# Optimization experiments

Measured on AMD Instinct MI355X. Metric: run time of the kernel, lower is better.

Reference implementation:

```python
import jax, jax.numpy as jnp
import numpy as np

L = 4        # num_layers
N = 50000    # nodes
E = 500000   # edges
B = 32       # graphs
H = 64       # hidden_dim
HP = 16      # hidden_dim_pe
P = 8        # pe_dim
BN_EPS = 1e-5


def setup_inputs() -> dict:
    key = jax.random.key(0)
    ks = jax.random.split(key, 22)
    nrm = lambda k, s: jax.random.normal(k, s, dtype=jnp.float32)
    w = lambda k, s: nrm(k, s) * 0.1
    return {
        'x': nrm(ks[0], (N, H)),
        'pe': nrm(ks[1], (N, P)),
        'Lambda': jax.random.uniform(ks[2], (B, P), dtype=jnp.float32),
        'edge_attr': nrm(ks[3], (E, H)),
        'edge_index': jax.random.randint(ks[4], (2, E), 0, N),
        'batch': jnp.sort(jax.random.randint(ks[5], (N,), 0, B)),
        # edge encoder (SPE): eigenvalue MLP + output projection
        'We1': w(ks[6], (L, P, HP * P)), 'be1': jnp.zeros((L, HP * P)),
        'Wee': w(ks[7], (L, HP, H)),     'bee': jnp.zeros((L, H)),
        # GINE mlp: Linear-BN-ReLU-Linear
        'W1': w(ks[8], (L, H, H)), 'b1': jnp.zeros((L, H)),
        'g1': jnp.ones((L, H)),    'beta1': jnp.zeros((L, H)),
        'W2': w(ks[9], (L, H, H)), 'b2': jnp.zeros((L, H)),
        # equivariant PE conv: edge gate + channel Linear
        'Wg': w(ks[10], (L, H, HP)),  'bg': jnp.zeros((L, HP)),
        'Wp': w(ks[11], (L, HP, HP)), 'bp': jnp.zeros((L, HP)),
        # outer BatchNorm per layer
        'gn': jnp.ones((L, H)), 'bnb': jnp.zeros((L, H)),
    }


def _bn(h, gamma, beta):
    mu = h.mean(0)
    var = h.var(0)
    return gamma * (h - mu) * jax.lax.rsqrt(var + BN_EPS) + beta


def reference(x, pe, Lambda, edge_attr, We1, be1, Wee, bee, W1, b1, g1, beta1,
              W2, b2, Wg, bg, Wp, bp, gn, bnb, edge_index, batch):
    src, dst = edge_index[0], edge_index[1]
    bsrc = batch[src]                       # [E] graph id of source node
    z = jnp.tile(pe[:, None, :], (1, HP, 1))  # [N, HP, P]
    for i in range(L):
        # SPE edge encoder: phi(Lambda)-weighted inner product over pe axis
        phi = jax.nn.relu(Lambda @ We1[i] + be1[i]).reshape(B, HP, P)
        eh = jnp.einsum('ehp,ehp->eh', phi[bsrc] * z[src], z[dst])  # [E, HP]
        ea = eh @ Wee[i] + bee[i] + edge_attr                       # [E, H]
        # GINEConv: scatter-add of relu(x_src + edge_attr), eps = 0
        agg = jax.ops.segment_sum(jax.nn.relu(x[src] + ea), dst, num_segments=N)
        h = x + agg
        h = jax.nn.relu(_bn(h @ W1[i] + b1[i], g1[i], beta1[i])) @ W2[i] + b2[i]
        # GINConvEquivariant: gated scatter-add, Linear on channel axis
        gate = jax.nn.relu(ea @ Wg[i] + bg[i])                      # [E, HP]
        msgz = jax.nn.relu(z[src] + gate[:, :, None])               # [E, HP, P]
        z = z + jax.ops.segment_sum(msgz, dst, num_segments=N)
        z = jnp.einsum('nhp,hk->nkp', z, Wp[i]) + bp[i][None, :, None]
        x = _bn(h, gn[i], bnb[i])
        if i != L - 1:
            x = jax.nn.relu(x)
    return x, z
```

## Files before the change

### kernel.cpp

```cpp
#include <hip/hip_runtime.h>

#define NN 50000
#define EE 500000
#define LL 4

typedef unsigned short u16;
typedef unsigned int u32;

__device__ __forceinline__ float bfc(u16 u) { return __uint_as_float(((u32)u) << 16); }
__device__ __forceinline__ u16 f2bf(float f) {
    u32 u = __float_as_uint(f);
    return (u16)((u + 0x7fffu + ((u >> 16) & 1u)) >> 16);
}
__device__ __forceinline__ float lanebc(float v, int l) {
    return __int_as_float(__builtin_amdgcn_readlane(__float_as_int(v), l));
}
__device__ __forceinline__ void unpack2(u32 w, float& lo, float& hi) {
    lo = __uint_as_float(w << 16);
    hi = __uint_as_float(w & 0xffff0000u);
}

__global__ __launch_bounds__(256) void k_init(const float* __restrict__ x, float* __restrict__ Xf,
                                              int* __restrict__ deg, int* __restrict__ cursor) {
    for (int i = blockIdx.x * 256 + threadIdx.x; i < NN * 64; i += gridDim.x * 256)
        Xf[i] = x[i];
    for (int i = blockIdx.x * 256 + threadIdx.x; i < NN; i += gridDim.x * 256) {
        deg[i] = 0;
        cursor[i] = 0;
    }
}

__global__ __launch_bounds__(128) void k_phi(const float* __restrict__ Lam, const float* __restrict__ We1,
                                             const float* __restrict__ be1, float* __restrict__ phiA) {
    int l = blockIdx.x >> 5, b = blockIdx.x & 31, j = threadIdx.x;
    float acc = be1[l * 128 + j];
    for (int q = 0; q < 8; q++)
        acc = fmaf(Lam[b * 8 + q], We1[l * 1024 + q * 128 + j], acc);
    phiA[l * 4096 + b * 128 + j] = fmaxf(acc, 0.f);
}

__global__ __launch_bounds__(256) void k_small(const float* __restrict__ Wee, const float* __restrict__ Wg,
                                               float* __restrict__ MA) {
    int l = blockIdx.x, t = threadIdx.x;
    int k = t >> 4, h = t & 15;
    float m = 0.f;
    for (int f = 0; f < 64; f++)
        m = fmaf(Wee[l * 1024 + k * 64 + f], Wg[l * 1024 + f * 16 + h], m);
    MA[l * 256 + t] = m;
}

__global__ __launch_bounds__(256) void k_hist(const int* __restrict__ ei, int* __restrict__ deg) {
    int e = blockIdx.x * 256 + threadIdx.x;
    if (e < EE) {
        int d = ei[EE + e];
        if (d >= 0 && d < NN) atomicAdd(&deg[d], 1);
    }
}

__global__ __launch_bounds__(256) void k_scan1(const int* __restrict__ deg, int* __restrict__ rowptr,
                                               int* __restrict__ bsum) {
    __shared__ int tmp[256];
    int t = threadIdx.x, i = blockIdx.x * 256 + t;
    int v = (i < NN) ? deg[i] : 0;
    tmp[t] = v;
    __syncthreads();
    for (int off = 1; off < 256; off <<= 1) {
        int a = (t >= off) ? tmp[t - off] : 0;
        __syncthreads();
        tmp[t] += a;
        __syncthreads();
    }
    if (i < NN) rowptr[i] = tmp[t] - v;
    if (t == 255) bsum[blockIdx.x] = tmp[255];
}

__global__ __launch_bounds__(256) void k_scan2(const int* __restrict__ bsum, int* __restrict__ boff,
                                               int* __restrict__ rowptr, int nb) {
    __shared__ int tmp[256];
    int t = threadIdx.x;
    int v = (t < nb) ? bsum[t] : 0;
    tmp[t] = v;
    __syncthreads();
    for (int off = 1; off < 256; off <<= 1) {
        int a = (t >= off) ? tmp[t - off] : 0;
        __syncthreads();
        tmp[t] += a;
        __syncthreads();
    }
    if (t < nb) boff[t] = tmp[t] - v;
    if (t == 255) rowptr[NN] = tmp[255];
}

__global__ __launch_bounds__(256) void k_scan3(int* __restrict__ rowptr, const int* __restrict__ boff) {
    int i = blockIdx.x * 256 + threadIdx.x;
    if (i < NN) rowptr[i] += boff[blockIdx.x];
}

__global__ __launch_bounds__(256) void k_scatter(const int* __restrict__ ei, const int* __restrict__ batch,
                                                 const int* __restrict__ rowptr, int* __restrict__ cursor,
                                                 u32* __restrict__ sb, int* __restrict__ eeo) {
    int e = blockIdx.x * 256 + threadIdx.x;
    if (e < EE) {
        int s = ei[e], d = ei[EE + e];
        if (s < 0) s = 0; if (s >= NN) s = NN - 1;
        if (d < 0) d = 0; if (d >= NN) d = NN - 1;
        int pos = rowptr[d] + atomicAdd(&cursor[d], 1);
        if (pos >= 0 && pos < EE) {
            sb[pos] = (u32)s | ((u32)(batch[s] & 31) << 16);
            eeo[pos] = e;
        }
    }
}

__global__ __launch_bounds__(256) void k_perm(const float* __restrict__ eat, const int* __restrict__ eeo,
                                              u16* __restrict__ eatp) {
    for (long long i = (long long)blockIdx.x * 256 + threadIdx.x; i < (long long)EE * 64;
         i += (long long)gridDim.x * 256) {
        int idx = (int)(i >> 6), j = (int)(i & 63);
        int e = eeo[idx];
        eatp[i] = f2bf(eat[(size_t)e * 64 + j]);
    }
}

__global__ __launch_bounds__(256) void k_eag2(const u16* __restrict__ eatp, const float* __restrict__ WgL,
                                              const float* __restrict__ beeL, const float* __restrict__ bgL,
                                              u32* __restrict__ EAGp) {
    __shared__ float sWg[1024];
    __shared__ float scv[16];
    __shared__ u32 srow[256][33];
    const int t = threadIdx.x;
    for (int i = t; i < 1024; i += 256) sWg[i] = WgL[i];
    __syncthreads();
    if (t < 16) {
        float c = bgL[t];
        for (int j = 0; j < 64; j++) c = fmaf(beeL[j], sWg[j * 16 + t], c);
        scv[t] = c;
    }
    const int base = blockIdx.x * 256;
    const u32* eat32 = (const u32*)eatp;
    for (int i = t; i < 256 * 32; i += 256) {
        int r = i >> 5, c = i & 31;
        int idx = base + r;
        srow[r][c] = (idx < EE) ? eat32[(size_t)idx * 32 + c] : 0u;
    }
    __syncthreads();
    const int idx = base + t;
    if (idx < EE) {
        float acc[16];
#pragma unroll
        for (int h = 0; h < 16; h++) acc[h] = scv[h];
#pragma unroll
        for (int c = 0; c < 32; c++) {
            float a0, a1;
            unpack2(srow[t][c], a0, a1);
            const float* w0 = &sWg[(2 * c) * 16];
#pragma unroll
            for (int h = 0; h < 16; h++) acc[h] = fmaf(a0, w0[h], fmaf(a1, w0[16 + h], acc[h]));
        }
        u32 w[8];
#pragma unroll
        for (int h = 0; h < 8; h++) w[h] = (u32)f2bf(acc[h]) | ((u32)f2bf(acc[8 + h]) << 16);
        uint4* op = reinterpret_cast<uint4*>(EAGp + (size_t)idx * 8);
        op[0] = make_uint4(w[0], w[1], w[2], w[3]);
        op[1] = make_uint4(w[4], w[5], w[6], w[7]);
    }
}

template <int INM>
__global__ __launch_bounds__(256) void k_edge_b(const float* __restrict__ Zf,
                                                const float* __restrict__ pe,
                                                const float* __restrict__ Xf,
                                                const u16* __restrict__ eatp, const u32* __restrict__ EAGp,
                                                const int* __restrict__ rowptr, const u32* __restrict__ sb,
                                                const float* __restrict__ phiL, const float* __restrict__ WeeL,
                                                const float* __restrict__ beeL, const float* __restrict__ ML,
                                                const float* __restrict__ WpL, const float* __restrict__ bpL,
                                                float* __restrict__ Hf, float* __restrict__ ZfO,
                                                double* __restrict__ stats) {
    __shared__ float sphi[32 * 128];
    __shared__ float sWp[256];
    __shared__ float sbp[16];
    if (blockIdx.x == 0) stats[threadIdx.x] = 0.0;
    for (int t = threadIdx.x; t < 4096; t += 256) sphi[t] = phiL[t];
    if (threadIdx.x < 256) sWp[threadIdx.x] = WpL[threadIdx.x];
    if (threadIdx.x < 16) sbp[threadIdx.x] = bpL[threadIdx.x];
    const int lane = threadIdx.x & 63;
    const int wid = threadIdx.x >> 6;
    const int hlo = lane >> 3;
    const int pp = lane & 7;
    float wee[16], mlo[16], mhi[16];
#pragma unroll
    for (int k = 0; k < 16; k++) {
        wee[k] = WeeL[k * 64 + lane];
        mlo[k] = ML[k * 16 + hlo];
        mhi[k] = ML[k * 16 + 8 + hlo];
    }
    const float beev = beeL[lane];
    __syncthreads();
    for (int n = blockIdx.x * 4 + wid; n < NN; n += gridDim.x * 4) {
        float zd0, zd1;
        if (INM == 0) { zd0 = zd1 = pe[n * 8 + pp]; }
        else { zd0 = Zf[n * 128 + lane]; zd1 = Zf[n * 128 + 64 + lane]; }
        float accx = Xf[n * 64 + lane];
        float az0 = zd0, az1 = zd1;
        int i0 = rowptr[n], i1 = rowptr[n + 1];
        if (i0 < 0) i0 = 0;
        if (i1 > EE) i1 = EE;
        u32 w = 0;
        float zs0 = 0.f, zs1 = 0.f, xs = 0.f, eav = 0.f, glo = 0.f, ghi = 0.f;
        if (i0 < i1) {
            w = sb[i0];
            const int s = w & 0xffff;
            if (INM == 0) { zs0 = zs1 = pe[s * 8 + pp]; }
            else { zs0 = Zf[s * 128 + lane]; zs1 = Zf[s * 128 + 64 + lane]; }
            xs = Xf[s * 64 + lane];
            eav = bfc(eatp[(size_t)i0 * 64 + lane]);
            unpack2(EAGp[(size_t)i0 * 8 + hlo], glo, ghi);
        }
        for (int idx = i0; idx < i1; ++idx) {
            const int idxn = (idx + 1 < i1) ? idx + 1 : idx;
            const u32 wn = sb[idxn];
            const int sn = wn & 0xffff;
            float zs0n, zs1n;
            if (INM == 0) { zs0n = zs1n = pe[sn * 8 + pp]; }
            else { zs0n = Zf[sn * 128 + lane]; zs1n = Zf[sn * 128 + 64 + lane]; }
            const float xsn = Xf[sn * 64 + lane];
            const float eavn = bfc(eatp[(size_t)idxn * 64 + lane]);
            float glon, ghin;
            unpack2(EAGp[(size_t)idxn * 8 + hlo], glon, ghin);
            const int b = (w >> 16) & 31;
            float p0 = sphi[b * 128 + lane] * zs0 * zd0;
            float p1 = sphi[b * 128 + 64 + lane] * zs1 * zd1;
            p0 += __shfl_xor(p0, 1); p1 += __shfl_xor(p1, 1);
            p0 += __shfl_xor(p0, 2); p1 += __shfl_xor(p1, 2);
            p0 += __shfl_xor(p0, 4); p1 += __shfl_xor(p1, 4);
            float eaA = 0.f, eaB = 0.f, gloA = glo, gloB = 0.f, ghiA = ghi, ghiB = 0.f;
#pragma unroll
            for (int k = 0; k < 8; k++) {
                const float ehk = lanebc(p0, k << 3);
                eaA = fmaf(ehk, wee[k], eaA);
                gloA = fmaf(ehk, mlo[k], gloA);
                ghiA = fmaf(ehk, mhi[k], ghiA);
            }
#pragma unroll
            for (int k = 0; k < 8; k++) {
                const float ehk = lanebc(p1, k << 3);
                eaB = fmaf(ehk, wee[8 + k], eaB);
                gloB = fmaf(ehk, mlo[8 + k], gloB);
                ghiB = fmaf(ehk, mhi[8 + k], ghiB);
            }
            accx += fmaxf(0.f, xs + (beev + eav + eaA + eaB));
            az0 += fmaxf(0.f, zs0 + fmaxf(gloA + gloB, 0.f));
            az1 += fmaxf(0.f, zs1 + fmaxf(ghiA + ghiB, 0.f));
            w = wn; zs0 = zs0n; zs1 = zs1n; xs = xsn; eav = eavn; glo = glon; ghi = ghin;
        }
        Hf[n * 64 + lane] = accx;
        float r0 = sbp[hlo], r1 = sbp[8 + hlo];
#pragma unroll
        for (int h = 0; h < 8; h++) {
            const float v = __shfl(az0, (h << 3) + pp);
            r0 = fmaf(v, sWp[h * 16 + hlo], r0);
            r1 = fmaf(v, sWp[h * 16 + 8 + hlo], r1);
        }
#pragma unroll
        for (int h = 0; h < 8; h++) {
            const float v = __shfl(az1, (h << 3) + pp);
            r0 = fmaf(v, sWp[(8 + h) * 16 + hlo], r0);
            r1 = fmaf(v, sWp[(8 + h) * 16 + 8 + hlo], r1);
        }
        ZfO[n * 128 + lane] = r0;
        ZfO[n * 128 + 64 + lane] = r1;
    }
}

template <int INM>
__global__ __launch_bounds__(256) void k_edge_s(const float* __restrict__ Zf,
                                                const float* __restrict__ pe,
                                                const float* __restrict__ Xf, const float* __restrict__ eat,
                                                const int* __restrict__ rowptr, const u32* __restrict__ sb,
                                                const int* __restrict__ eeo,
                                                const float* __restrict__ phiL, const float* __restrict__ WeeL,
                                                const float* __restrict__ beeL,
                                                const float* __restrict__ WgL, const float* __restrict__ bgL,
                                                const float* __restrict__ WpL, const float* __restrict__ bpL,
                                                float* __restrict__ Hf, float* __restrict__ ZfO,
                                                double* __restrict__ stats) {
    __shared__ float sphi[32 * 128];
    __shared__ float sWp[256];
    __shared__ float sbp[16];
    if (blockIdx.x == 0) stats[threadIdx.x] = 0.0;
    for (int t = threadIdx.x; t < 4096; t += 256) sphi[t] = phiL[t];
    if (threadIdx.x < 256) sWp[threadIdx.x] = WpL[threadIdx.x];
    if (threadIdx.x < 16) sbp[threadIdx.x] = bpL[threadIdx.x];
    const int lane = threadIdx.x & 63;
    const int wid = threadIdx.x >> 6;
    const int hlo = lane >> 3;
    const int pp = lane & 7;
    const int h16 = lane & 15;
    const int g16 = lane & 48;
    float wee[16], wgr[16];
#pragma unroll
    for (int k = 0; k < 16; k++) {
        wee[k] = WeeL[k * 64 + lane];
        wgr[k] = WgL[(g16 + k) * 16 + h16];
    }
    const float beev = beeL[lane];
    const float bgr = bgL[h16];
    __syncthreads();
    for (int n = blockIdx.x * 4 + wid; n < NN; n += gridDim.x * 4) {
        float zd0, zd1;
        if (INM == 0) { zd0 = zd1 = pe[n * 8 + pp]; }
        else { zd0 = Zf[n * 128 + lane]; zd1 = Zf[n * 128 + 64 + lane]; }
        float accx = Xf[n * 64 + lane];
        float az0 = zd0, az1 = zd1;
        int i0 = rowptr[n], i1 = rowptr[n + 1];
        if (i0 < 0) i0 = 0;
        if (i1 > EE) i1 = EE;
        for (int idx = i0; idx < i1; ++idx) {
            const u32 w = sb[idx];
            const int s = w & 0xffff;
            const int b = (w >> 16) & 31;
            int e = eeo[idx];
            e = (e < 0) ? 0 : ((e >= EE) ? EE - 1 : e);
            float zs0, zs1;
            if (INM == 0) { zs0 = zs1 = pe[s * 8 + pp]; }
            else { zs0 = Zf[s * 128 + lane]; zs1 = Zf[s * 128 + 64 + lane]; }
            float p0 = sphi[b * 128 + lane] * zs0 * zd0;
            float p1 = sphi[b * 128 + 64 + lane] * zs1 * zd1;
            p0 += __shfl_xor(p0, 1); p1 += __shfl_xor(p1, 1);
            p0 += __shfl_xor(p0, 2); p1 += __shfl_xor(p1, 2);
            p0 += __shfl_xor(p0, 4); p1 += __shfl_xor(p1, 4);
            float ea = beev + eat[(size_t)e * 64 + lane];
#pragma unroll
            for (int k = 0; k < 8; k++) ea = fmaf(lanebc(p0, k << 3), wee[k], ea);
#pragma unroll
            for (int k = 0; k < 8; k++) ea = fmaf(lanebc(p1, k << 3), wee[8 + k], ea);
            float gp = 0.f;
#pragma unroll
            for (int i = 0; i < 16; i++) gp = fmaf(__shfl(ea, g16 + i), wgr[i], gp);
            gp += __shfl_xor(gp, 16);
            gp += __shfl_xor(gp, 32);
            const float gv = fmaxf(gp + bgr, 0.f);
            const float glo = __shfl(gv, hlo);
            const float ghi = __shfl(gv, 8 + hlo);
            const float xs = Xf[s * 64 + lane];
            accx += fmaxf(0.f, xs + ea);
            az0 += fmaxf(0.f, zs0 + glo);
            az1 += fmaxf(0.f, zs1 + ghi);
        }
        Hf[n * 64 + lane] = accx;
        float r0 = sbp[hlo], r1 = sbp[8 + hlo];
#pragma unroll
        for (int h = 0; h < 8; h++) {
            const float v = __shfl(az0, (h << 3) + pp);
            r0 = fmaf(v, sWp[h * 16 + hlo], r0);
            r1 = fmaf(v, sWp[h * 16 + 8 + hlo], r1);
        }
#pragma unroll
        for (int h = 0; h < 8; h++) {
            const float v = __shfl(az1, (h << 3) + pp);
            r0 = fmaf(v, sWp[(8 + h) * 16 + hlo], r0);
            r1 = fmaf(v, sWp[(8 + h) * 16 + 8 + hlo], r1);
        }
        ZfO[n * 128 + lane] = r0;
        ZfO[n * 128 + 64 + lane] = r1;
    }
}

__global__ __launch_bounds__(256) void k_gemm1(float* Buf, const float* __restrict__ WL,
                                               const float* __restrict__ bL,
                                               double* __restrict__ sum, double* __restrict__ sq) {
    __shared__ float sW[4096];
    __shared__ double red[512];
    for (int t = threadIdx.x; t < 4096; t += 256) sW[t] = WL[t];
    const int lane = threadIdx.x & 63, wid = threadIdx.x >> 6;
    const float bv = bL[lane];
    __syncthreads();
    double s = 0.0, q = 0.0;
    for (int n = blockIdx.x * 4 + wid; n < NN; n += gridDim.x * 4) {
        const float h = Buf[n * 64 + lane];
        float acc = bv;
#pragma unroll
        for (int k = 0; k < 64; k++) acc = fmaf(lanebc(h, k), sW[k * 64 + lane], acc);
        Buf[n * 64 + lane] = acc;
        s += (double)acc;
        q += (double)acc * (double)acc;
    }
    red[threadIdx.x] = s;
    red[256 + threadIdx.x] = q;
    __syncthreads();
    if (threadIdx.x < 64) {
        s = red[threadIdx.x] + red[threadIdx.x + 64] + red[threadIdx.x + 128] + red[threadIdx.x + 192];
        q = red[256 + threadIdx.x] + red[320 + threadIdx.x] + red[384 + threadIdx.x] + red[448 + threadIdx.x];
        atomicAdd(&sum[lane], s);
        atomicAdd(&sq[lane], q);
    }
}

__global__ __launch_bounds__(256) void k_gemm2(float* Buf, const float* __restrict__ WL,
                                               const float* __restrict__ bL,
                                               const float* __restrict__ gL, const float* __restrict__ betaL,
                                               const double* __restrict__ s1, const double* __restrict__ q1,
                                               double* __restrict__ sum, double* __restrict__ sq) {
    __shared__ float sW[4096];
    __shared__ double red[512];
    for (int t = threadIdx.x; t < 4096; t += 256) sW[t] = WL[t];
    const int lane = threadIdx.x & 63, wid = threadIdx.x >> 6;
    const float bv = bL[lane];
    const double mu = s1[lane] * (1.0 / NN);
    const double var = q1[lane] * (1.0 / NN) - mu * mu;
    const float inv = rsqrtf(fmaxf((float)var, 0.f) + 1e-5f);
    const float gm = gL[lane] * inv;
    const float ga = betaL[lane] - (float)mu * gm;
    __syncthreads();
    double s = 0.0, q = 0.0;
    for (int n = blockIdx.x * 4 + wid; n < NN; n += gridDim.x * 4) {
        const float v = Buf[n * 64 + lane];
        const float r = fmaxf(fmaf(v, gm, ga), 0.f);
        float acc = bv;
#pragma unroll
        for (int k = 0; k < 64; k++) acc = fmaf(lanebc(r, k), sW[k * 64 + lane], acc);
        Buf[n * 64 + lane] = acc;
        s += (double)acc;
        q += (double)acc * (double)acc;
    }
    red[threadIdx.x] = s;
    red[256 + threadIdx.x] = q;
    __syncthreads();
    if (threadIdx.x < 64) {
        s = red[threadIdx.x] + red[threadIdx.x + 64] + red[threadIdx.x + 128] + red[threadIdx.x + 192];
        q = red[256 + threadIdx.x] + red[320 + threadIdx.x] + red[384 + threadIdx.x] + red[448 + threadIdx.x];
        atomicAdd(&sum[lane], s);
        atomicAdd(&sq[lane], q);
    }
}

__global__ __launch_bounds__(256) void k_bnout(const float* __restrict__ In, float* __restrict__ Xf,
                                               const double* __restrict__ s2, const double* __restrict__ q2,
                                               const float* __restrict__ gL, const float* __restrict__ bL,
                                               int dorelu) {
    int i = blockIdx.x * 256 + threadIdx.x;
    const int f = i & 63;
    const double mu = s2[f] * (1.0 / NN);
    const double var = q2[f] * (1.0 / NN) - mu * mu;
    const float inv = rsqrtf(fmaxf((float)var, 0.f) + 1e-5f);
    const float gm = gL[f] * inv;
    const float ga = bL[f] - (float)mu * gm;
    for (; i < NN * 64; i += gridDim.x * 256) {
        float o = fmaf(In[i], gm, ga);
        if (dorelu) o = fmaxf(o, 0.f);
        Xf[i] = o;
    }
}

extern "C" void kernel_launch(void* const* d_in, const int* in_sizes, int n_in,
                              void* d_out, int out_size, void* d_ws, size_t ws_size,
                              hipStream_t stream) {
    (void)in_sizes; (void)n_in; (void)out_size;
    const float* x    = (const float*)d_in[0];
    const float* pe   = (const float*)d_in[1];
    const float* Lam  = (const float*)d_in[2];
    const float* eat  = (const float*)d_in[3];
    const int*   ei   = (const int*)d_in[4];
    const int*   batch= (const int*)d_in[5];
    const float* We1  = (const float*)d_in[6];
    const float* be1  = (const float*)d_in[7];
    const float* Wee  = (const float*)d_in[8];
    const float* bee  = (const float*)d_in[9];
    const float* W1   = (const float*)d_in[10];
    const float* b1   = (const float*)d_in[11];
    const float* g1   = (const float*)d_in[12];
    const float* bt1  = (const float*)d_in[13];
    const float* W2   = (const float*)d_in[14];
    const float* b2   = (const float*)d_in[15];
    const float* Wg   = (const float*)d_in[16];
    const float* bg   = (const float*)d_in[17];
    const float* Wp   = (const float*)d_in[18];
    const float* bp   = (const float*)d_in[19];
    const float* gn   = (const float*)d_in[20];
    const float* bnb  = (const float*)d_in[21];

    float* Xf = (float*)d_out;
    float* B  = (float*)d_out + 3200000;

    float* A    = (float*)d_ws;
    float* Hf   = A + 6400000;
    float* MA   = Hf + 3200000;
    float* phiA = MA + 1024;
    double* stats = (double*)(phiA + 16384);
    double* s1 = stats, *q1 = stats + 64, *s2 = stats + 128, *q2 = stats + 192;
    int* rowptr = (int*)(stats + 256);
    int* deg    = rowptr + NN + 1;
    int* bsum   = deg + NN;
    int* boff   = bsum + 256;
    int* cursor = boff + 256;
    u32* sb     = (u32*)(cursor + NN);
    int* eeo    = (int*)(sb + EE);
    u32* EAGp   = (u32*)(eeo + EE);
    u16* eatp   = (u16*)(EAGp + (size_t)EE * 8);
    const size_t NEED_BIG = (size_t)((char*)(eatp + (size_t)EE * 64) - (char*)d_ws);
    const bool big = (ws_size >= NEED_BIG);

    const int NB_N = (NN + 255) / 256;
    const int NB_E = (EE + 255) / 256;

    k_init<<<1024, 256, 0, stream>>>(x, Xf, deg, cursor);
    k_phi<<<LL * 32, 128, 0, stream>>>(Lam, We1, be1, phiA);
    k_hist<<<NB_E, 256, 0, stream>>>(ei, deg);
    k_scan1<<<NB_N, 256, 0, stream>>>(deg, rowptr, bsum);
    k_scan2<<<1, 256, 0, stream>>>(bsum, boff, rowptr, NB_N);
    k_scan3<<<NB_N, 256, 0, stream>>>(rowptr, boff);
    k_scatter<<<NB_E, 256, 0, stream>>>(ei, batch, rowptr, cursor, sb, eeo);
    if (big) {
        k_small<<<LL, 256, 0, stream>>>(Wee, Wg, MA);
        k_perm<<<8192, 256, 0, stream>>>(eat, eeo, eatp);
    }

    for (int l = 0; l < LL; l++) {
        const float* WeeL = Wee + l * 1024;
        const float* beeL = bee + l * 64;
        const float* WgL  = Wg + l * 1024;
        const float* bgL  = bg + l * 16;
        const float* WpL  = Wp + l * 256;
        const float* bpL  = bp + l * 16;
        const float* phiL = phiA + l * 4096;
        const float* Zin  = (l == 2) ? B : A;
        float*       Zout = (l == 1 || l == 3) ? B : A;
        if (big) {
            k_eag2<<<NB_E, 256, 0, stream>>>(eatp, WgL, beeL, bgL, EAGp);
            if (l == 0)
                k_edge_b<0><<<6272, 256, 0, stream>>>(nullptr, pe, Xf, eatp, EAGp, rowptr, sb,
                                                      phiL, WeeL, beeL, MA + l * 256, WpL, bpL,
                                                      Hf, Zout, stats);
            else
                k_edge_b<1><<<6272, 256, 0, stream>>>(Zin, pe, Xf, eatp, EAGp, rowptr, sb,
                                                      phiL, WeeL, beeL, MA + l * 256, WpL, bpL,
                                                      Hf, Zout, stats);
        } else {
            if (l == 0)
                k_edge_s<0><<<2048, 256, 0, stream>>>(nullptr, pe, Xf, eat, rowptr, sb, eeo,
                                                      phiL, WeeL, beeL, WgL, bgL, WpL, bpL,
                                                      Hf, Zout, stats);
            else
                k_edge_s<1><<<2048, 256, 0, stream>>>(Zin, pe, Xf, eat, rowptr, sb, eeo,
                                                      phiL, WeeL, beeL, WgL, bgL, WpL, bpL,
                                                      Hf, Zout, stats);
        }
        k_gemm1<<<512, 256, 0, stream>>>(Hf, W1 + l * 4096, b1 + l * 64, s1, q1);
        k_gemm2<<<512, 256, 0, stream>>>(Hf, W2 + l * 4096, b2 + l * 64,
                                         g1 + l * 64, bt1 + l * 64, s1, q1, s2, q2);
        k_bnout<<<1024, 256, 0, stream>>>(Hf, Xf, s2, q2, gn + l * 64, bnb + l * 64,
                                          (l == LL - 1) ? 0 : 1);
    }
}
```

Before: 1.244 ms.

## Store node features in bf16, batch edge loads per 64-edge chunk, vectorize permute

Node features X are now kept in bf16 between layers, which halves the gather traffic in the edge kernel. The edge kernel loads source indices for 64 edges at once, broadcasts them with readlane, and software-pipelines two edges per step. Z is stored interleaved as float2 so one load covers both halves. Other changes: k_perm uses float4 loads, the GEMM dot products are split into two accumulators, and a new BN output kernel writes bf16 X. The cost is extra rounding of activations to bf16 and more register pressure in the edge loop.

```diff
diff --git a/kernel.cpp b/kernel.cpp
--- a/kernel.cpp
+++ b/kernel.cpp
@@ -21,9 +21,12 @@
 }
 
 __global__ __launch_bounds__(256) void k_init(const float* __restrict__ x, float* __restrict__ Xf,
+                                              u16* __restrict__ Xh, int big,
                                               int* __restrict__ deg, int* __restrict__ cursor) {
-    for (int i = blockIdx.x * 256 + threadIdx.x; i < NN * 64; i += gridDim.x * 256)
-        Xf[i] = x[i];
+    for (int i = blockIdx.x * 256 + threadIdx.x; i < NN * 64; i += gridDim.x * 256) {
+        if (big) Xh[i] = f2bf(x[i]);
+        else Xf[i] = x[i];
+    }
     for (int i = blockIdx.x * 256 + threadIdx.x; i < NN; i += gridDim.x * 256) {
         deg[i] = 0;
         cursor[i] = 0;
@@ -114,11 +117,16 @@
 
 __global__ __launch_bounds__(256) void k_perm(const float* __restrict__ eat, const int* __restrict__ eeo,
                                               u16* __restrict__ eatp) {
-    for (long long i = (long long)blockIdx.x * 256 + threadIdx.x; i < (long long)EE * 64;
+    const float4* e4 = reinterpret_cast<const float4*>(eat);
+    ushort4* o4 = reinterpret_cast<ushort4*>(eatp);
+    for (long long i = (long long)blockIdx.x * 256 + threadIdx.x; i < (long long)EE * 16;
          i += (long long)gridDim.x * 256) {
-        int idx = (int)(i >> 6), j = (int)(i & 63);
+        int idx = (int)(i >> 4), cc = (int)(i & 15);
         int e = eeo[idx];
-        eatp[i] = f2bf(eat[(size_t)e * 64 + j]);
+        float4 v = e4[(size_t)e * 16 + cc];
+        ushort4 o;
+        o.x = f2bf(v.x); o.y = f2bf(v.y); o.z = f2bf(v.z); o.w = f2bf(v.w);
+        o4[i] = o;
     }
 }
 
@@ -166,18 +174,50 @@
     }
 }
 
-template <int INM>
-__global__ __launch_bounds__(256) void k_edge_b(const float* __restrict__ Zf,
-                                                const float* __restrict__ pe,
-                                                const float* __restrict__ Xf,
-                                                const u16* __restrict__ eatp, const u32* __restrict__ EAGp,
-                                                const int* __restrict__ rowptr, const u32* __restrict__ sb,
-                                                const float* __restrict__ phiL, const float* __restrict__ WeeL,
-                                                const float* __restrict__ beeL, const float* __restrict__ ML,
-                                                const float* __restrict__ WpL, const float* __restrict__ bpL,
-                                                float* __restrict__ Hf, float* __restrict__ ZfO,
-                                                double* __restrict__ stats) {
-    __shared__ float sphi[32 * 128];
+#define EF(P, kk) do { \
+    P##w = (u32)__builtin_amdgcn_readlane((int)svec, (kk)); \
+    int s_ = (int)(P##w & 0xffffu); \
+    if (INM == 0) { P##z0 = P##z1 = pe[s_ * 8 + pp]; } \
+    else { float2 t_ = Z2[s_ * 64 + lane]; P##z0 = t_.x; P##z1 = t_.y; } \
+    P##xs = bfc(Xh[s_ * 64 + lane]); \
+    size_t ge_ = (size_t)(c + (kk)); \
+    P##ea = bfc(eatp[ge_ * 64 + lane]); \
+    unpack2(EAGp[ge_ * 8 + hlo], P##gl, P##gh); \
+} while (0)
+
+#define EC(P, MSK) do { \
+    int b_ = (int)((P##w >> 16) & 31u); \
+    float p0 = sphi[b_ * 128 + lane] * P##z0 * zd0; \
+    float p1 = sphi[b_ * 128 + 64 + lane] * P##z1 * zd1; \
+    p0 += __shfl_xor(p0, 1); p1 += __shfl_xor(p1, 1); \
+    p0 += __shfl_xor(p0, 2); p1 += __shfl_xor(p1, 2); \
+    p0 += __shfl_xor(p0, 4); p1 += __shfl_xor(p1, 4); \
+    float eaA = 0.f, eaB = 0.f, gA = P##gl, gB = 0.f, hA = P##gh, hB = 0.f; \
+    _Pragma("unroll") \
+    for (int k_ = 0; k_ < 8; k_++) { float e_ = lanebc(p0, k_ << 3); \
+        eaA = fmaf(e_, wee[k_], eaA); gA = fmaf(e_, mlo[k_], gA); hA = fmaf(e_, mhi[k_], hA); } \
+    _Pragma("unroll") \
+    for (int k_ = 0; k_ < 8; k_++) { float e_ = lanebc(p1, k_ << 3); \
+        eaB = fmaf(e_, wee[8 + k_], eaB); gB = fmaf(e_, mlo[8 + k_], gB); hB = fmaf(e_, mhi[8 + k_], hB); } \
+    float ea_ = beev + P##ea + eaA + eaB; \
+    accx = fmaf(MSK, fmaxf(0.f, P##xs + ea_), accx); \
+    az0  = fmaf(MSK, fmaxf(0.f, P##z0 + fmaxf(gA + gB, 0.f)), az0); \
+    az1  = fmaf(MSK, fmaxf(0.f, P##z1 + fmaxf(hA + hB, 0.f)), az1); \
+} while (0)
+
+template <int INM, int FIN>
+__global__ __launch_bounds__(256) void k_edge2(const float2* __restrict__ Z2,
+                                               const float* __restrict__ pe,
+                                               const u16* __restrict__ Xh,
+                                               const u16* __restrict__ eatp, const u32* __restrict__ EAGp,
+                                               const int* __restrict__ rowptr, const u32* __restrict__ sb,
+                                               const float* __restrict__ phiL, const float* __restrict__ WeeL,
+                                               const float* __restrict__ beeL, const float* __restrict__ ML,
+                                               const float* __restrict__ WpL, const float* __restrict__ bpL,
+                                               float* __restrict__ Hf, float2* __restrict__ Z2O,
+                                               float* __restrict__ outz,
+                                               double* __restrict__ stats) {
+    __shared__ float sphi[4096];
     __shared__ float sWp[256];
     __shared__ float sbp[16];
     if (blockIdx.x == 0) stats[threadIdx.x] = 0.0;
@@ -200,59 +240,35 @@
     for (int n = blockIdx.x * 4 + wid; n < NN; n += gridDim.x * 4) {
         float zd0, zd1;
         if (INM == 0) { zd0 = zd1 = pe[n * 8 + pp]; }
-        else { zd0 = Zf[n * 128 + lane]; zd1 = Zf[n * 128 + 64 + lane]; }
-        float accx = Xf[n * 64 + lane];
+        else { float2 t = Z2[n * 64 + lane]; zd0 = t.x; zd1 = t.y; }
+        float accx = bfc(Xh[n * 64 + lane]);
         float az0 = zd0, az1 = zd1;
         int i0 = rowptr[n], i1 = rowptr[n + 1];
         if (i0 < 0) i0 = 0;
         if (i1 > EE) i1 = EE;
-        u32 w = 0;
-        float zs0 = 0.f, zs1 = 0.f, xs = 0.f, eav = 0.f, glo = 0.f, ghi = 0.f;
-        if (i0 < i1) {
-            w = sb[i0];
-            const int s = w & 0xffff;
-            if (INM == 0) { zs0 = zs1 = pe[s * 8 + pp]; }
-            else { zs0 = Zf[s * 128 + lane]; zs1 = Zf[s * 128 + 64 + lane]; }
-            xs = Xf[s * 64 + lane];
-            eav = bfc(eatp[(size_t)i0 * 64 + lane]);
-            unpack2(EAGp[(size_t)i0 * 8 + hlo], glo, ghi);
-        }
-        for (int idx = i0; idx < i1; ++idx) {
-            const int idxn = (idx + 1 < i1) ? idx + 1 : idx;
-            const u32 wn = sb[idxn];
-            const int sn = wn & 0xffff;
-            float zs0n, zs1n;
-            if (INM == 0) { zs0n = zs1n = pe[sn * 8 + pp]; }
-            else { zs0n = Zf[sn * 128 + lane]; zs1n = Zf[sn * 128 + 64 + lane]; }
-            const float xsn = Xf[sn * 64 + lane];
-            const float eavn = bfc(eatp[(size_t)idxn * 64 + lane]);
-            float glon, ghin;
-            unpack2(EAGp[(size_t)idxn * 8 + hlo], glon, ghin);
-            const int b = (w >> 16) & 31;
-            float p0 = sphi[b * 128 + lane] * zs0 * zd0;
-            float p1 = sphi[b * 128 + 64 + lane] * zs1 * zd1;
-            p0 += __shfl_xor(p0, 1); p1 += __shfl_xor(p1, 1);
-            p0 += __shfl_xor(p0, 2); p1 += __shfl_xor(p1, 2);
-            p0 += __shfl_xor(p0, 4); p1 += __shfl_xor(p1, 4);
-            float eaA = 0.f, eaB = 0.f, gloA = glo, gloB = 0.f, ghiA = ghi, ghiB = 0.f;
-#pragma unroll
-            for (int k = 0; k < 8; k++) {
-                const float ehk = lanebc(p0, k << 3);
-                eaA = fmaf(ehk, wee[k], eaA);
-                gloA = fmaf(ehk, mlo[k], gloA);
-                ghiA = fmaf(ehk, mhi[k], ghiA);
+        for (int c = i0; c < i1; c += 64) {
+            const int ce = (c + 64 < i1) ? c + 64 : i1;
+            const int m = ce - c;
+            const int mL = m - 1;
+            int ci = c + lane; if (ci > i1 - 1) ci = i1 - 1;
+            const u32 svec = sb[ci];
+            u32 Aw, Bw, Nw, Mw;
+            float Az0, Az1, Axs, Aea, Agl, Agh;
+            float Bz0, Bz1, Bxs, Bea, Bgl, Bgh;
+            float Nz0, Nz1, Nxs, Nea, Ngl, Ngh;
+            float Mz0, Mz1, Mxs, Mea, Mgl, Mgh;
+            EF(A, 0);
+            EF(B, (1 > mL ? mL : 1));
+            for (int k = 0; k < m; k += 2) {
+                const int n0 = (k + 2 > mL) ? mL : k + 2;
+                const int n1 = (k + 3 > mL) ? mL : k + 3;
+                EF(N, n0);
+                EF(M, n1);
+                EC(A, 1.f);
+                EC(B, (k + 1 <= mL) ? 1.f : 0.f);
+                Aw = Nw; Az0 = Nz0; Az1 = Nz1; Axs = Nxs; Aea = Nea; Agl = Ngl; Agh = Ngh;
+                Bw = Mw; Bz0 = Mz0; Bz1 = Mz1; Bxs = Mxs; Bea = Mea; Bgl = Mgl; Bgh = Mgh;
             }
-#pragma unroll
-            for (int k = 0; k < 8; k++) {
-                const float ehk = lanebc(p1, k << 3);
-                eaB = fmaf(ehk, wee[8 + k], eaB);
-                gloB = fmaf(ehk, mlo[8 + k], gloB);
-                ghiB = fmaf(ehk, mhi[8 + k], ghiB);
-            }
-            accx += fmaxf(0.f, xs + (beev + eav + eaA + eaB));
-            az0 += fmaxf(0.f, zs0 + fmaxf(gloA + gloB, 0.f));
-            az1 += fmaxf(0.f, zs1 + fmaxf(ghiA + ghiB, 0.f));
-            w = wn; zs0 = zs0n; zs1 = zs1n; xs = xsn; eav = eavn; glo = glon; ghi = ghin;
         }
         Hf[n * 64 + lane] = accx;
         float r0 = sbp[hlo], r1 = sbp[8 + hlo];
@@ -268,8 +284,12 @@
             r0 = fmaf(v, sWp[(8 + h) * 16 + hlo], r0);
             r1 = fmaf(v, sWp[(8 + h) * 16 + 8 + hlo], r1);
         }
-        ZfO[n * 128 + lane] = r0;
-        ZfO[n * 128 + 64 + lane] = r1;
+        if (FIN) {
+            outz[n * 128 + lane] = r0;
+            outz[n * 128 + 64 + lane] = r1;
+        } else {
+            Z2O[n * 64 + lane] = make_float2(r0, r1);
+        }
     }
 }
 
@@ -379,9 +399,12 @@
     double s = 0.0, q = 0.0;
     for (int n = blockIdx.x * 4 + wid; n < NN; n += gridDim.x * 4) {
         const float h = Buf[n * 64 + lane];
-        float acc = bv;
-#pragma unroll
-        for (int k = 0; k < 64; k++) acc = fmaf(lanebc(h, k), sW[k * 64 + lane], acc);
+        float a0 = bv, a1 = 0.f;
+#pragma unroll
+        for (int k = 0; k < 32; k++) a0 = fmaf(lanebc(h, k), sW[k * 64 + lane], a0);
+#pragma unroll
+        for (int k = 32; k < 64; k++) a1 = fmaf(lanebc(h, k), sW[k * 64 + lane], a1);
+        const float acc = a0 + a1;
         Buf[n * 64 + lane] = acc;
         s += (double)acc;
         q += (double)acc * (double)acc;
@@ -417,9 +440,12 @@
     for (int n = blockIdx.x * 4 + wid; n < NN; n += gridDim.x * 4) {
         const float v = Buf[n * 64 + lane];
         const float r = fmaxf(fmaf(v, gm, ga), 0.f);
-        float acc = bv;
-#pragma unroll
-        for (int k = 0; k < 64; k++) acc = fmaf(lanebc(r, k), sW[k * 64 + lane], acc);
+        float a0 = bv, a1 = 0.f;
+#pragma unroll
+        for (int k = 0; k < 32; k++) a0 = fmaf(lanebc(r, k), sW[k * 64 + lane], a0);
+#pragma unroll
+        for (int k = 32; k < 64; k++) a1 = fmaf(lanebc(r, k), sW[k * 64 + lane], a1);
+        const float acc = a0 + a1;
         Buf[n * 64 + lane] = acc;
         s += (double)acc;
         q += (double)acc * (double)acc;
@@ -432,6 +458,29 @@
         q = red[256 + threadIdx.x] + red[320 + threadIdx.x] + red[384 + threadIdx.x] + red[448 + threadIdx.x];
         atomicAdd(&sum[lane], s);
         atomicAdd(&sq[lane], q);
+    }
+}
+
+__global__ __launch_bounds__(256) void k_bnout2(const float* __restrict__ In, u16* __restrict__ Xh,
+                                                float* __restrict__ outx,
+                                                const double* __restrict__ s2, const double* __restrict__ q2,
+                                                const float* __restrict__ gL, const float* __restrict__ bL,
+                                                int last) {
+    int i = blockIdx.x * 256 + threadIdx.x;
+    const int f = i & 63;
+    const double mu = s2[f] * (1.0 / NN);
+    const double var = q2[f] * (1.0 / NN) - mu * mu;
+    const float inv = rsqrtf(fmaxf((float)var, 0.f) + 1e-5f);
+    const float gm = gL[f] * inv;
+    const float ga = bL[f] - (float)mu * gm;
+    for (; i < NN * 64; i += gridDim.x * 256) {
+        float o = fmaf(In[i], gm, ga);
+        if (last) {
+            outx[i] = o;
+        } else {
+            o = fmaxf(o, 0.f);
+            Xh[i] = f2bf(o);
+        }
     }
 }
 
@@ -480,8 +529,9 @@
     const float* gn   = (const float*)d_in[20];
     const float* bnb  = (const float*)d_in[21];
 
-    float* Xf = (float*)d_out;
-    float* B  = (float*)d_out + 3200000;
+    float* Xf   = (float*)d_out;
+    u16*   Xh   = (u16*)d_out;
+    float* B    = (float*)d_out + 3200000;
 
     float* A    = (float*)d_ws;
     float* Hf   = A + 6400000;
@@ -501,10 +551,13 @@
     const size_t NEED_BIG = (size_t)((char*)(eatp + (size_t)EE * 64) - (char*)d_ws);
     const bool big = (ws_size >= NEED_BIG);
 
+    float2* A2 = (float2*)A;
+    float2* B2 = (float2*)B;
+
     const int NB_N = (NN + 255) / 256;
     const int NB_E = (EE + 255) / 256;
 
-    k_init<<<1024, 256, 0, stream>>>(x, Xf, deg, cursor);
+    k_init<<<1024, 256, 0, stream>>>(x, Xf, Xh, big ? 1 : 0, deg, cursor);
     k_phi<<<LL * 32, 128, 0, stream>>>(Lam, We1, be1, phiA);
     k_hist<<<NB_E, 256, 0, stream>>>(ei, deg);
     k_scan1<<<NB_N, 256, 0, stream>>>(deg, rowptr, bsum);
@@ -513,7 +566,7 @@
     k_scatter<<<NB_E, 256, 0, stream>>>(ei, batch, rowptr, cursor, sb, eeo);
     if (big) {
         k_small<<<LL, 256, 0, stream>>>(Wee, Wg, MA);
-        k_perm<<<8192, 256, 0, stream>>>(eat, eeo, eatp);
+        k_perm<<<4096, 256, 0, stream>>>(eat, eeo, eatp);
     }
 
     for (int l = 0; l < LL; l++) {
@@ -524,19 +577,28 @@
         const float* WpL  = Wp + l * 256;
         const float* bpL  = bp + l * 16;
         const float* phiL = phiA + l * 4096;
-        const float* Zin  = (l == 2) ? B : A;
-        float*       Zout = (l == 1 || l == 3) ? B : A;
+        const float* ML   = MA + l * 256;
         if (big) {
             k_eag2<<<NB_E, 256, 0, stream>>>(eatp, WgL, beeL, bgL, EAGp);
             if (l == 0)
-                k_edge_b<0><<<6272, 256, 0, stream>>>(nullptr, pe, Xf, eatp, EAGp, rowptr, sb,
-                                                      phiL, WeeL, beeL, MA + l * 256, WpL, bpL,
-                                                      Hf, Zout, stats);
+                k_edge2<0, 0><<<6272, 256, 0, stream>>>(A2, pe, Xh, eatp, EAGp, rowptr, sb,
+                                                        phiL, WeeL, beeL, ML, WpL, bpL,
+                                                        Hf, A2, nullptr, stats);
+            else if (l == 1)
+                k_edge2<1, 0><<<6272, 256, 0, stream>>>(A2, pe, Xh, eatp, EAGp, rowptr, sb,
+                                                        phiL, WeeL, beeL, ML, WpL, bpL,
+                                                        Hf, B2, nullptr, stats);
+            else if (l == 2)
+                k_edge2<1, 0><<<6272, 256, 0, stream>>>(B2, pe, Xh, eatp, EAGp, rowptr, sb,
+                                                        phiL, WeeL, beeL, ML, WpL, bpL,
+                                                        Hf, A2, nullptr, stats);
             else
-                k_edge_b<1><<<6272, 256, 0, stream>>>(Zin, pe, Xf, eatp, EAGp, rowptr, sb,
-                                                      phiL, WeeL, beeL, MA + l * 256, WpL, bpL,
-                                                      Hf, Zout, stats);
+                k_edge2<1, 1><<<6272, 256, 0, stream>>>(A2, pe, Xh, eatp, EAGp, rowptr, sb,
+                                                        phiL, WeeL, beeL, ML, WpL, bpL,
+                                                        Hf, nullptr, B, stats);
         } else {
+            const float* Zin  = (l == 2) ? B : A;
+            float*       Zout = (l == 1 || l == 3) ? B : A;
             if (l == 0)
                 k_edge_s<0><<<2048, 256, 0, stream>>>(nullptr, pe, Xf, eat, rowptr, sb, eeo,
                                                       phiL, WeeL, beeL, WgL, bgL, WpL, bpL,
@@ -549,7 +611,11 @@
         k_gemm1<<<512, 256, 0, stream>>>(Hf, W1 + l * 4096, b1 + l * 64, s1, q1);
         k_gemm2<<<512, 256, 0, stream>>>(Hf, W2 + l * 4096, b2 + l * 64,
                                          g1 + l * 64, bt1 + l * 64, s1, q1, s2, q2);
-        k_bnout<<<1024, 256, 0, stream>>>(Hf, Xf, s2, q2, gn + l * 64, bnb + l * 64,
-                                          (l == LL - 1) ? 0 : 1);
-    }
-}
+        if (big)
+            k_bnout2<<<1024, 256, 0, stream>>>(Hf, Xh, Xf, s2, q2, gn + l * 64, bnb + l * 64,
+                                               (l == LL - 1) ? 1 : 0);
+        else
+            k_bnout<<<1024, 256, 0, stream>>>(Hf, Xf, s2, q2, gn + l * 64, bnb + l * 64,
+                                              (l == LL - 1) ? 0 : 1);
+    }
+}
```

New measurement: 1.117 ms. 1.11x faster.
